# Kernel optimization log

Measured on AMD Instinct MI355X. Metric: run time of the kernel, lower is better.

Reference implementation:

```python
import jax, jax.numpy as jnp
import numpy as np

DIM = 512  # word_hidden_size * 2


def _linear_params(key, din, dout, scale=0.05):
    kw, kb = jax.random.split(key)
    W = jax.random.normal(kw, (din, dout), dtype=jnp.float32) * scale
    b = jax.random.normal(kb, (dout,), dtype=jnp.float32) * scale
    return W, b


def setup_inputs() -> dict:
    key = jax.random.key(0)
    ks = jax.random.split(key, 16)
    S_c, S_q, B = 256, 32, 32
    inp = {
        'context_output': jax.random.normal(ks[0], (S_c, B, DIM), dtype=jnp.float32),
        'question_output': jax.random.normal(ks[1], (S_q, B, DIM), dtype=jnp.float32),
        'question_hidden_state': jax.random.normal(ks[2], (B, DIM), dtype=jnp.float32),
        'image_output': jax.random.normal(ks[3], (S_c, B, DIM), dtype=jnp.float32),
    }
    names = ['fc1', 'fc2', 'dm', 'rm', 'qm', 'rr', 'rg', 'qg']
    for i, n in enumerate(names):
        W, b = _linear_params(ks[4 + i], DIM, DIM)
        inp['W_' + n] = W
        inp['b_' + n] = b
    W_ms, b_ms = _linear_params(ks[12], DIM, 1)
    inp['W_ms'] = W_ms
    inp['b_ms'] = b_ms
    return inp


def reference(context_output, question_output, question_hidden_state, image_output,
              W_fc1, b_fc1, W_fc2, b_fc2, W_dm, b_dm, W_rm, b_rm, W_qm, b_qm,
              W_rr, b_rr, W_rg, b_rg, W_qg, b_qg, W_ms, b_ms):
    # ctx: [B, S, D] = fc1(context) + fc2(image) after seq-first -> batch-first permute
    ctx = (jnp.einsum('sbd,de->bse', context_output, W_fc1) + b_fc1
           + jnp.einsum('sbd,de->bse', image_output, W_fc2) + b_fc2)
    # hoist loop-invariant linear_dm(ctx): same math, computed once
    ctx_dm = jnp.einsum('bsd,de->bse', ctx, W_dm) + b_dm  # [B, S, D]

    B = ctx.shape[0]
    r0 = jnp.zeros((B, DIM), dtype=ctx.dtype)

    def step(r, q_t):  # r: [B, D], q_t: [B, D]
        rm = r @ W_rm + b_rm          # [B, D]
        qm = q_t @ W_qm + b_qm        # [B, D]
        m = jnp.tanh(ctx_dm + rm[:, None, :] + qm[:, None, :])  # [B, S, D]
        logits = jnp.einsum('bsd,do->bso', m, W_ms)[..., 0] + b_ms[0]  # [B, S]
        s = jax.nn.softmax(logits, axis=1)                     # [B, S]
        r_new = jnp.einsum('bs,bsd->bd', s, ctx) + jnp.tanh(r @ W_rr + b_rr)
        return r_new, None

    r, _ = jax.lax.scan(step, r0, question_output)  # scan over question tokens

    g = (r @ W_rg + b_rg) + (question_hidden_state @ W_qg + b_qg)  # [B, D]
    return g
```

## Files before the change

### kernel.cpp

```cpp
#include <hip/hip_runtime.h>
#include <hip/hip_bf16.h>

#define DIMD 512
#define NB   32
#define NS   256
#define NT   32
#define SA_STR  66
#define SCT_STR 258
#define SR_STR  132

typedef __bf16 bf16x8 __attribute__((ext_vector_type(8)));
typedef float  f32x4  __attribute__((ext_vector_type(4)));
typedef unsigned long long u64;

__device__ __forceinline__ float tanh_fast(float x) {
    float e = __expf(2.f * x);
    return 1.f - 2.f / (e + 1.f);
}

__device__ __forceinline__ void gl_lds16(const __bf16* g, __bf16* l) {
    __builtin_amdgcn_global_load_lds((const __attribute__((address_space(1))) void*)g,
                                     (__attribute__((address_space(3))) void*)l, 16, 0, 0);
}

__device__ __forceinline__ void pub64(u64* p, float v, unsigned tag) {
    u64 pk = ((u64)__float_as_uint(v) << 32) | (u64)tag;
    __hip_atomic_store(p, pk, __ATOMIC_RELAXED, __HIP_MEMORY_SCOPE_AGENT);
}
__device__ __forceinline__ float poll64(const u64* p, unsigned tag) {
    u64 v = __hip_atomic_load(p, __ATOMIC_RELAXED, __HIP_MEMORY_SCOPE_AGENT);
    while ((unsigned)v != tag) {
        __builtin_amdgcn_s_sleep(1);
        v = __hip_atomic_load(p, __ATOMIC_RELAXED, __HIP_MEMORY_SCOPE_AGENT);
    }
    return __uint_as_float((unsigned)(v >> 32));
}

__global__ void k_prep_all(const float* __restrict__ ctxin, const float* __restrict__ img,
                           const float* __restrict__ qin,
                           const float* __restrict__ Wfc1, const float* __restrict__ Wfc2,
                           const float* __restrict__ Wdm, const float* __restrict__ Wqm,
                           const float* __restrict__ Wrm, const float* __restrict__ Wrr,
                           const float* __restrict__ Wrg, const float* __restrict__ Wqg,
                           __bf16* __restrict__ acat, __bf16* __restrict__ qp,
                           __bf16* __restrict__ wcatT, __bf16* __restrict__ wdmT,
                           __bf16* __restrict__ wqmT, __bf16* __restrict__ wrmT,
                           __bf16* __restrict__ wrrT, __bf16* __restrict__ wrgT,
                           __bf16* __restrict__ wqgT) {
    int row = blockIdx.x;
    if (row < 8192) {
        int b = row >> 8, s = row & 255;
        const float* c  = ctxin + ((size_t)s * NB + b) * DIMD;
        const float* im = img   + ((size_t)s * NB + b) * DIMD;
        __bf16* o = acat + (size_t)row * 1024;
        for (int d = threadIdx.x; d < DIMD; d += 256) {
            o[d]       = (__bf16)c[d];
            o[512 + d] = (__bf16)im[d];
        }
    } else if (row < 10240) {
        int idx = (row - 8192) * 256 + threadIdx.x;
        qp[idx] = (__bf16)qin[idx];
    } else {
        __shared__ float tile[32][33];
        int zz = (row - 10240) >> 8;
        int idx = (row - 10240) & 255;
        int bx = idx & 15, by = idx >> 4;
        int x = threadIdx.x & 31, y = threadIdx.x >> 5;
        const float* src = (zz == 0) ? Wfc1 : (zz == 1) ? Wfc2 : (zz == 2) ? Wdm
                         : (zz == 3) ? Wqm : (zz == 4) ? Wrm : (zz == 5) ? Wrr
                         : (zz == 6) ? Wrg : Wqg;
        __bf16* dst; int stride, off;
        if (zz < 2) { dst = wcatT; stride = 1024; off = zz * 512; }
        else {
            dst = (zz == 2) ? wdmT : (zz == 3) ? wqmT : (zz == 4) ? wrmT
                : (zz == 5) ? wrrT : (zz == 6) ? wrgT : wqgT;
            stride = 512; off = 0;
        }
        int c0 = bx * 32, r0 = by * 32;
#pragma unroll
        for (int k = 0; k < 32; k += 8)
            tile[y + k][x] = src[(size_t)(r0 + y + k) * DIMD + c0 + x];
        __syncthreads();
#pragma unroll
        for (int k = 0; k < 32; k += 8)
            dst[(size_t)(c0 + y + k) * stride + off + r0 + x] = (__bf16)tile[x][y + k];
    }
}

__device__ __forceinline__ void gemm_tile(const __bf16* __restrict__ A,
                                          const __bf16* __restrict__ BT,
                                          const float* __restrict__ bias1,
                                          const float* __restrict__ bias2,
                                          void* __restrict__ out, int N, int K,
                                          int m0, int n0, int out_f32,
                                          __bf16* As, __bf16* Bs) {
    int tid = threadIdx.x, wave = tid >> 6, lane = tid & 63;
    int wm = wave >> 1, wn = wave & 1;
    int lr = lane & 15, lq = lane >> 4;

    f32x4 acc[2][2];
#pragma unroll
    for (int i = 0; i < 2; i++)
#pragma unroll
        for (int j = 0; j < 2; j++) acc[i][j] = (f32x4){0.f, 0.f, 0.f, 0.f};

    int g0 = (wave * 2 + 0) * 64 + lane;
    int g1 = (wave * 2 + 1) * 64 + lane;
    int r0_ = g0 >> 3, c0_ = g0 & 7;
    int r1_ = g1 >> 3, c1_ = g1 & 7;
    __bf16* la0 = As + (wave * 2 + 0) * 512;
    __bf16* la1 = As + (wave * 2 + 1) * 512;
    __bf16* lb0 = Bs + (wave * 2 + 0) * 512;
    __bf16* lb1 = Bs + (wave * 2 + 1) * 512;

    for (int kk = 0; kk < K; kk += 64) {
        gl_lds16(A  + (size_t)(m0 + r0_) * K + kk + c0_ * 8, la0);
        gl_lds16(A  + (size_t)(m0 + r1_) * K + kk + c1_ * 8, la1);
        gl_lds16(BT + (size_t)(n0 + r0_) * K + kk + c0_ * 8, lb0);
        gl_lds16(BT + (size_t)(n0 + r1_) * K + kk + c1_ * 8, lb1);
        __syncthreads();
#pragma unroll
        for (int k2 = 0; k2 < 64; k2 += 32) {
            bf16x8 af[2], bfv[2];
#pragma unroll
            for (int i = 0; i < 2; i++)
                af[i] = *(const bf16x8*)(As + (wm * 32 + i * 16 + lr) * 64 + k2 + lq * 8);
#pragma unroll
            for (int j = 0; j < 2; j++)
                bfv[j] = *(const bf16x8*)(Bs + (wn * 32 + j * 16 + lr) * 64 + k2 + lq * 8);
#pragma unroll
            for (int i = 0; i < 2; i++)
#pragma unroll
                for (int j = 0; j < 2; j++)
                    acc[i][j] = __builtin_amdgcn_mfma_f32_16x16x32_bf16(af[i], bfv[j], acc[i][j], 0, 0, 0);
        }
        __syncthreads();
    }

#pragma unroll
    for (int i = 0; i < 2; i++)
#pragma unroll
        for (int j = 0; j < 2; j++) {
            int col = n0 + wn * 32 + j * 16 + lr;
            float bs = (bias1 ? bias1[col] : 0.f) + (bias2 ? bias2[col] : 0.f);
#pragma unroll
            for (int r = 0; r < 4; r++) {
                int row = m0 + wm * 32 + i * 16 + lq * 4 + r;
                float v = acc[i][j][r] + bs;
                if (out_f32) ((float*)out)[(size_t)row * N + col] = v;
                else         ((__bf16*)out)[(size_t)row * N + col] = (__bf16)v;
            }
        }
}

__global__ void k_gemm64(const __bf16* __restrict__ A, const __bf16* __restrict__ BT,
                         const float* __restrict__ bias1, const float* __restrict__ bias2,
                         void* __restrict__ out, int M, int N, int K, int out_f32) {
    __shared__ __bf16 As[64 * 64];
    __shared__ __bf16 Bs[64 * 64];
    gemm_tile(A, BT, bias1, bias2, out, N, K, blockIdx.x * 64, blockIdx.y * 64, out_f32, As, Bs);
}

__global__ void k_fused(const __bf16* __restrict__ ctxb, const __bf16* __restrict__ wdmT,
                        const float* __restrict__ bdm, __bf16* __restrict__ ctxdm,
                        const __bf16* __restrict__ qp, const __bf16* __restrict__ wqmT,
                        const float* __restrict__ bqm, float* __restrict__ qmf,
                        __bf16* __restrict__ ctxT) {
    __shared__ __bf16 As[64 * 64];
    __shared__ __bf16 Bs[64 * 64];
    int bid = blockIdx.x;
    if (bid < 1024) {
        gemm_tile(ctxb, wdmT, bdm, nullptr, ctxdm, 512, 512,
                  (bid & 127) * 64, (bid >> 7) * 64, 0, As, Bs);
    } else if (bid < 1152) {
        int b2 = bid - 1024;
        gemm_tile(qp, wqmT, bqm, nullptr, qmf, 512, 512,
                  (b2 & 15) * 64, (b2 >> 4) * 64, 1, As, Bs);
    } else {
        int b3 = bid - 1152;
        int z = b3 >> 7, rest = b3 & 127;
        int c0 = (rest & 15) * 32, s0 = (rest >> 4) * 32;
        __bf16* tile = As;
        int x = threadIdx.x & 31, y = threadIdx.x >> 5;
        const __bf16* S = ctxb + (size_t)z * NS * DIMD;
        __bf16* D = ctxT + (size_t)z * DIMD * NS;
#pragma unroll
        for (int k = 0; k < 32; k += 8)
            tile[(y + k) * 33 + x] = S[(size_t)(s0 + y + k) * DIMD + c0 + x];
        __syncthreads();
#pragma unroll
        for (int k = 0; k < 32; k += 8)
            D[(size_t)(c0 + y + k) * NS + s0 + x] = tile[x * 33 + y + k];
    }
}

__global__ __launch_bounds__(512, 2) void k_scan(
    const __bf16* __restrict__ ctxdm,
    const __bf16* __restrict__ ctxT,
    const __bf16* __restrict__ wrmT,
    const __bf16* __restrict__ wrrT,
    const float* __restrict__ qmf,
    const float* __restrict__ wms, const float* __restrict__ brm,
    const float* __restrict__ brr,
    u64* parts,
    u64* rpub,
    float* __restrict__ rbuf) {
    int bid = blockIdx.x;
    int b = bid & 31, j = bid >> 5;
    int tid = threadIdx.x, wave = tid >> 6, lane = tid & 63;
    int g = lane >> 3, i = lane & 7;

    __shared__ __bf16 sA[256 * SA_STR];
    __shared__ __bf16 sCT[64 * SCT_STR];
    __shared__ float  sQ[NT * 64];
    __shared__ float  sq[512];
    __shared__ float  sp[256];
    __shared__ float  s4[4];
    __shared__ float  sps[8 * 68];
    __shared__ float  srm[64], sh[64];
    __shared__ float  sr4[4 * SR_STR];
    __shared__ float  smv[512];

    for (int c = tid; c < 2048; c += 512) {
        int row = c >> 3, c8 = c & 7;
        *(bf16x8*)(sA + row * SA_STR + c8 * 8) =
            *(const bf16x8*)(ctxdm + ((size_t)(b * NS + row)) * DIMD + j * 64 + c8 * 8);
    }
    for (int c = tid; c < 2048; c += 512) {
        int col = c >> 5, s8 = c & 31;
        *(bf16x8*)(sCT + col * SCT_STR + s8 * 8) =
            *(const bf16x8*)(ctxT + ((size_t)(b * DIMD) + j * 64 + col) * NS + s8 * 8);
    }
    for (int c = tid; c < NT * 64; c += 512) {
        int tt = c >> 6, e = c & 63;
        sQ[c] = qmf[((size_t)tt * NB + b) * DIMD + j * 64 + e];
    }
    int m = tid >> 8, cl = (tid >> 2) & 63, q = tid & 3;
    const __bf16* wp = (m ? wrrT : wrmT) + ((size_t)(j * 64 + cl)) * DIMD + q * 128;
    bf16x8 wreg[16];
#pragma unroll
    for (int u = 0; u < 16; u++) wreg[u] = *(const bf16x8*)(wp + u * 8);

    float wm[8];
#pragma unroll
    for (int u = 0; u < 8; u++) wm[u] = wms[j * 64 + i * 8 + u];
    if (tid < 64) {
        srm[tid] = brm[j * 64 + tid];
        sh[tid]  = tanh_fast(brr[j * 64 + tid]);
    }
    __syncthreads();

    for (int t = 0; t < NT; t++) {
        unsigned tag = (unsigned)(t + 1);
        float rq[8];
#pragma unroll
        for (int u = 0; u < 8; u++) rq[u] = srm[i * 8 + u] + sQ[t * 64 + i * 8 + u];
#pragma unroll
        for (int k = 0; k < 4; k++) {
            int s = wave * 32 + k * 8 + g;
            bf16x8 cv = *(const bf16x8*)(sA + s * SA_STR + i * 8);
            float a = 0.f;
#pragma unroll
            for (int u = 0; u < 8; u++)
                a += tanh_fast((float)cv[u] + rq[u]) * wm[u];
            a += __shfl_xor(a, 1); a += __shfl_xor(a, 2); a += __shfl_xor(a, 4);
            if (i == 0) pub64(&parts[(b * 8 + j) * NS + s], a, tag);
        }

        {
            int s = tid >> 1, jh = (tid & 1) * 4;
            const u64* p0 = &parts[(b * 8 + jh + 0) * NS + s];
            const u64* p1 = &parts[(b * 8 + jh + 1) * NS + s];
            const u64* p2 = &parts[(b * 8 + jh + 2) * NS + s];
            const u64* p3 = &parts[(b * 8 + jh + 3) * NS + s];
            u64 v0, v1, v2, v3;
            for (;;) {
                v0 = __hip_atomic_load(p0, __ATOMIC_RELAXED, __HIP_MEMORY_SCOPE_AGENT);
                v1 = __hip_atomic_load(p1, __ATOMIC_RELAXED, __HIP_MEMORY_SCOPE_AGENT);
                v2 = __hip_atomic_load(p2, __ATOMIC_RELAXED, __HIP_MEMORY_SCOPE_AGENT);
                v3 = __hip_atomic_load(p3, __ATOMIC_RELAXED, __HIP_MEMORY_SCOPE_AGENT);
                if ((unsigned)v0 == tag && (unsigned)v1 == tag &&
                    (unsigned)v2 == tag && (unsigned)v3 == tag) break;
                __builtin_amdgcn_s_sleep(1);
            }
            sq[tid] = __uint_as_float((unsigned)(v0 >> 32)) + __uint_as_float((unsigned)(v1 >> 32))
                    + __uint_as_float((unsigned)(v2 >> 32)) + __uint_as_float((unsigned)(v3 >> 32));
        }
        __syncthreads();
        float ev = 0.f;
        if (tid < NS) { ev = __expf(sq[2 * tid] + sq[2 * tid + 1]); sp[tid] = ev; }
#pragma unroll
        for (int off = 32; off; off >>= 1) ev += __shfl_xor(ev, off);
        if (tid < NS && lane == 0) s4[wave] = ev;
        __syncthreads();
        float inv = 1.f / (s4[0] + s4[1] + s4[2] + s4[3]);
        {
            const __bf16* cp = sCT + lane * SCT_STR + wave * 32;
            const float* pp = sp + wave * 32;
            float a = 0.f;
#pragma unroll
            for (int k = 0; k < 32; k += 8) {
                bf16x8 v = *(const bf16x8*)(cp + k);
#pragma unroll
                for (int u = 0; u < 8; u++) a = fmaf(pp[k + u], (float)v[u], a);
            }
            sps[wave * 68 + lane] = a;
        }
        __syncthreads();
        if (tid < 64) {
            float a = 0.f;
#pragma unroll
            for (int w2 = 0; w2 < 8; w2++) a += sps[w2 * 68 + tid];
            float rv = a * inv + sh[tid];
            if (t == NT - 1) rbuf[b * DIMD + j * 64 + tid] = rv;
            else             pub64(&rpub[b * DIMD + j * 64 + tid], rv, tag);
        }
        if (t == NT - 1) break;

        sr4[(tid >> 7) * SR_STR + (tid & 127)] = poll64(&rpub[b * DIMD + tid], tag);
        __syncthreads();
        {
            const float* sv = sr4 + q * SR_STR;
            float a0 = 0.f, a1 = 0.f;
#pragma unroll
            for (int u = 0; u < 16; u += 2) {
                bf16x8 w0 = wreg[u], w1 = wreg[u + 1];
#pragma unroll
                for (int e = 0; e < 8; e++) {
                    a0 = fmaf(sv[u * 8 + e],     (float)w0[e], a0);
                    a1 = fmaf(sv[u * 8 + 8 + e], (float)w1[e], a1);
                }
            }
            smv[tid] = a0 + a1;
        }
        __syncthreads();
        if (tid < 128) {
            int m2 = tid >> 6, cl3 = tid & 63;
            float a = smv[m2 * 256 + cl3 * 4] + smv[m2 * 256 + cl3 * 4 + 1]
                    + smv[m2 * 256 + cl3 * 4 + 2] + smv[m2 * 256 + cl3 * 4 + 3];
            int col = j * 64 + cl3;
            if (m2 == 0) srm[cl3] = a + brm[col];
            else         sh[cl3]  = tanh_fast(a + brr[col]);
        }
        __syncthreads();
    }
}

__global__ void k_final2(const float* __restrict__ r, const float* __restrict__ qh,
                         const __bf16* __restrict__ wrgT, const __bf16* __restrict__ wqgT,
                         const float* __restrict__ brg, const float* __restrict__ bqg,
                         float* __restrict__ out) {
    int clx = threadIdx.x & 7, b = threadIdx.x >> 3;
    int col = blockIdx.x * 8 + clx;
    const __bf16* w1 = wrgT + (size_t)col * DIMD;
    const __bf16* w2 = wqgT + (size_t)col * DIMD;
    const float* rp = r + (size_t)b * DIMD;
    const float* qp = qh + (size_t)b * DIMD;
    float acc = brg[col] + bqg[col];
#pragma unroll 4
    for (int d = 0; d < DIMD; d += 8) {
        bf16x8 a = *(const bf16x8*)(w1 + d);
        bf16x8 c = *(const bf16x8*)(w2 + d);
#pragma unroll
        for (int u = 0; u < 8; u++)
            acc += rp[d + u] * (float)a[u] + qp[d + u] * (float)c[u];
    }
    out[b * DIMD + col] = acc;
}


extern "C" void kernel_launch(void* const* d_in, const int* in_sizes, int n_in,
                              void* d_out, int out_size, void* d_ws, size_t ws_size,
                              hipStream_t stream) {
    const float* ctx_in = (const float*)d_in[0];
    const float* q_in   = (const float*)d_in[1];
    const float* qh     = (const float*)d_in[2];
    const float* img    = (const float*)d_in[3];
    const float* W_fc1  = (const float*)d_in[4];
    const float* b_fc1  = (const float*)d_in[5];
    const float* W_fc2  = (const float*)d_in[6];
    const float* b_fc2  = (const float*)d_in[7];
    const float* W_dm   = (const float*)d_in[8];
    const float* b_dm   = (const float*)d_in[9];
    const float* W_rm   = (const float*)d_in[10];
    const float* b_rm   = (const float*)d_in[11];
    const float* W_qm   = (const float*)d_in[12];
    const float* b_qm   = (const float*)d_in[13];
    const float* W_rr   = (const float*)d_in[14];
    const float* b_rr   = (const float*)d_in[15];
    const float* W_rg   = (const float*)d_in[16];
    const float* b_rg   = (const float*)d_in[17];
    const float* W_qg   = (const float*)d_in[18];
    const float* b_qg   = (const float*)d_in[19];
    const float* W_ms   = (const float*)d_in[20];

    char* w = (char*)d_ws;
    __bf16* acat  = (__bf16*)w;  w += (size_t)8192 * 1024 * 2;
    __bf16* qp    = (__bf16*)w;  w += (size_t)1024 * 512 * 2;
    __bf16* wcatT = (__bf16*)w;  w += (size_t)512 * 1024 * 2;
    __bf16* wdmT  = (__bf16*)w;  w += (size_t)512 * 512 * 2;
    __bf16* wqmT  = (__bf16*)w;  w += (size_t)512 * 512 * 2;
    __bf16* wrmT  = (__bf16*)w;  w += (size_t)512 * 512 * 2;
    __bf16* wrrT  = (__bf16*)w;  w += (size_t)512 * 512 * 2;
    __bf16* wrgT  = (__bf16*)w;  w += (size_t)512 * 512 * 2;
    __bf16* wqgT  = (__bf16*)w;  w += (size_t)512 * 512 * 2;
    __bf16* ctxb  = (__bf16*)w;  w += (size_t)8192 * 512 * 2;
    __bf16* ctxdm = (__bf16*)w;  w += (size_t)8192 * 512 * 2;
    char* x = (char*)acat;
    __bf16* ctxT  = (__bf16*)x;  x += (size_t)NB * DIMD * NS * 2;
    float*  qmf   = (float*)x;   x += (size_t)1024 * 512 * 4;
    u64*    rpub  = (u64*)x;     x += (size_t)NB * DIMD * 8;
    u64*    parts = (u64*)x;     x += (size_t)NB * 8 * NS * 8;
    float*  rbuf  = (float*)x;   x += (size_t)NB * DIMD * 4;

    k_prep_all<<<12288, 256, 0, stream>>>(ctx_in, img, q_in, W_fc1, W_fc2, W_dm,
                                          W_qm, W_rm, W_rr, W_rg, W_qg, acat, qp,
                                          wcatT, wdmT, wqmT, wrmT, wrrT, wrgT, wqgT);
    k_gemm64<<<dim3(128, 8), 256, 0, stream>>>(acat, wcatT, b_fc1, b_fc2, ctxb, 8192, 512, 1024, 0);
    k_fused<<<5248, 256, 0, stream>>>(ctxb, wdmT, b_dm, ctxdm, qp, wqmT, b_qm, qmf, ctxT);
    k_scan<<<256, 512, 0, stream>>>(ctxdm, ctxT, wrmT, wrrT, qmf, W_ms,
                                    b_rm, b_rr, parts, rpub, rbuf);
    k_final2<<<64, 256, 0, stream>>>(rbuf, qh, wrgT, wqgT, b_rg, b_qg, (float*)d_out);
}
```

Baseline: 447.7 us.

## Use 128x128 GEMM tiles and fold final gate projection into scan kernel

GEMM tiles grow from 64x64 (K step 64) to 128x128 (K step 32), so each wave does 4x4 MFMA blocks. This raises operand reuse per LDS load and cuts the block count for the fc and dm/qm GEMMs. Separately, the last scan step now publishes r and computes the rg/qg output projection inside k_scan, which removes the k_final2 launch and the round-trip through rbuf. The cost is more registers per thread for the accumulators, fewer blocks (256 for the main GEMM) to fill the CUs, and extra weight loads in the scan's final step.

```diff
diff --git a/kernel.cpp b/kernel.cpp
--- a/kernel.cpp
+++ b/kernel.cpp
@@ -87,65 +87,62 @@
     }
 }
 
-__device__ __forceinline__ void gemm_tile(const __bf16* __restrict__ A,
-                                          const __bf16* __restrict__ BT,
-                                          const float* __restrict__ bias1,
-                                          const float* __restrict__ bias2,
-                                          void* __restrict__ out, int N, int K,
-                                          int m0, int n0, int out_f32,
-                                          __bf16* As, __bf16* Bs) {
+__device__ __forceinline__ void gemm_tile128(const __bf16* __restrict__ A,
+                                             const __bf16* __restrict__ BT,
+                                             const float* __restrict__ bias1,
+                                             const float* __restrict__ bias2,
+                                             void* __restrict__ out, int N, int K,
+                                             int m0, int n0, int out_f32,
+                                             __bf16* As, __bf16* Bs) {
     int tid = threadIdx.x, wave = tid >> 6, lane = tid & 63;
-    int wm = wave >> 1, wn = wave & 1;
+    int wm_ = wave >> 1, wn = wave & 1;
     int lr = lane & 15, lq = lane >> 4;
 
-    f32x4 acc[2][2];
-#pragma unroll
-    for (int i = 0; i < 2; i++)
-#pragma unroll
-        for (int j = 0; j < 2; j++) acc[i][j] = (f32x4){0.f, 0.f, 0.f, 0.f};
+    f32x4 acc[4][4];
+#pragma unroll
+    for (int i = 0; i < 4; i++)
+#pragma unroll
+        for (int j = 0; j < 4; j++) acc[i][j] = (f32x4){0.f, 0.f, 0.f, 0.f};
 
     int g0 = (wave * 2 + 0) * 64 + lane;
     int g1 = (wave * 2 + 1) * 64 + lane;
-    int r0_ = g0 >> 3, c0_ = g0 & 7;
-    int r1_ = g1 >> 3, c1_ = g1 & 7;
+    int r0_ = g0 >> 2, c0_ = g0 & 3;
+    int r1_ = g1 >> 2, c1_ = g1 & 3;
     __bf16* la0 = As + (wave * 2 + 0) * 512;
     __bf16* la1 = As + (wave * 2 + 1) * 512;
     __bf16* lb0 = Bs + (wave * 2 + 0) * 512;
     __bf16* lb1 = Bs + (wave * 2 + 1) * 512;
 
-    for (int kk = 0; kk < K; kk += 64) {
+    for (int kk = 0; kk < K; kk += 32) {
         gl_lds16(A  + (size_t)(m0 + r0_) * K + kk + c0_ * 8, la0);
         gl_lds16(A  + (size_t)(m0 + r1_) * K + kk + c1_ * 8, la1);
         gl_lds16(BT + (size_t)(n0 + r0_) * K + kk + c0_ * 8, lb0);
         gl_lds16(BT + (size_t)(n0 + r1_) * K + kk + c1_ * 8, lb1);
         __syncthreads();
-#pragma unroll
-        for (int k2 = 0; k2 < 64; k2 += 32) {
-            bf16x8 af[2], bfv[2];
-#pragma unroll
-            for (int i = 0; i < 2; i++)
-                af[i] = *(const bf16x8*)(As + (wm * 32 + i * 16 + lr) * 64 + k2 + lq * 8);
-#pragma unroll
-            for (int j = 0; j < 2; j++)
-                bfv[j] = *(const bf16x8*)(Bs + (wn * 32 + j * 16 + lr) * 64 + k2 + lq * 8);
-#pragma unroll
-            for (int i = 0; i < 2; i++)
-#pragma unroll
-                for (int j = 0; j < 2; j++)
-                    acc[i][j] = __builtin_amdgcn_mfma_f32_16x16x32_bf16(af[i], bfv[j], acc[i][j], 0, 0, 0);
-        }
-        __syncthreads();
-    }
-
-#pragma unroll
-    for (int i = 0; i < 2; i++)
-#pragma unroll
-        for (int j = 0; j < 2; j++) {
-            int col = n0 + wn * 32 + j * 16 + lr;
+        bf16x8 af[4], bfv[4];
+#pragma unroll
+        for (int i = 0; i < 4; i++)
+            af[i] = *(const bf16x8*)(As + (wm_ * 64 + i * 16 + lr) * 32 + lq * 8);
+#pragma unroll
+        for (int j = 0; j < 4; j++)
+            bfv[j] = *(const bf16x8*)(Bs + (wn * 64 + j * 16 + lr) * 32 + lq * 8);
+#pragma unroll
+        for (int i = 0; i < 4; i++)
+#pragma unroll
+            for (int j = 0; j < 4; j++)
+                acc[i][j] = __builtin_amdgcn_mfma_f32_16x16x32_bf16(af[i], bfv[j], acc[i][j], 0, 0, 0);
+        __syncthreads();
+    }
+
+#pragma unroll
+    for (int i = 0; i < 4; i++)
+#pragma unroll
+        for (int j = 0; j < 4; j++) {
+            int col = n0 + wn * 64 + j * 16 + lr;
             float bs = (bias1 ? bias1[col] : 0.f) + (bias2 ? bias2[col] : 0.f);
 #pragma unroll
             for (int r = 0; r < 4; r++) {
-                int row = m0 + wm * 32 + i * 16 + lq * 4 + r;
+                int row = m0 + wm_ * 64 + i * 16 + lq * 4 + r;
                 float v = acc[i][j][r] + bs;
                 if (out_f32) ((float*)out)[(size_t)row * N + col] = v;
                 else         ((__bf16*)out)[(size_t)row * N + col] = (__bf16)v;
@@ -153,12 +150,12 @@
         }
 }
 
-__global__ void k_gemm64(const __bf16* __restrict__ A, const __bf16* __restrict__ BT,
-                         const float* __restrict__ bias1, const float* __restrict__ bias2,
-                         void* __restrict__ out, int M, int N, int K, int out_f32) {
-    __shared__ __bf16 As[64 * 64];
-    __shared__ __bf16 Bs[64 * 64];
-    gemm_tile(A, BT, bias1, bias2, out, N, K, blockIdx.x * 64, blockIdx.y * 64, out_f32, As, Bs);
+__global__ void k_gemm128(const __bf16* __restrict__ A, const __bf16* __restrict__ BT,
+                          const float* __restrict__ bias1, const float* __restrict__ bias2,
+                          void* __restrict__ out, int M, int N, int K, int out_f32) {
+    __shared__ __bf16 As[128 * 32];
+    __shared__ __bf16 Bs[128 * 32];
+    gemm_tile128(A, BT, bias1, bias2, out, N, K, blockIdx.x * 128, blockIdx.y * 128, out_f32, As, Bs);
 }
 
 __global__ void k_fused(const __bf16* __restrict__ ctxb, const __bf16* __restrict__ wdmT,
@@ -166,18 +163,18 @@
                         const __bf16* __restrict__ qp, const __bf16* __restrict__ wqmT,
                         const float* __restrict__ bqm, float* __restrict__ qmf,
                         __bf16* __restrict__ ctxT) {
-    __shared__ __bf16 As[64 * 64];
-    __shared__ __bf16 Bs[64 * 64];
+    __shared__ __bf16 As[128 * 32];
+    __shared__ __bf16 Bs[128 * 32];
     int bid = blockIdx.x;
-    if (bid < 1024) {
-        gemm_tile(ctxb, wdmT, bdm, nullptr, ctxdm, 512, 512,
-                  (bid & 127) * 64, (bid >> 7) * 64, 0, As, Bs);
-    } else if (bid < 1152) {
-        int b2 = bid - 1024;
-        gemm_tile(qp, wqmT, bqm, nullptr, qmf, 512, 512,
-                  (b2 & 15) * 64, (b2 >> 4) * 64, 1, As, Bs);
+    if (bid < 256) {
+        gemm_tile128(ctxb, wdmT, bdm, nullptr, ctxdm, 512, 512,
+                     (bid & 63) * 128, (bid >> 6) * 128, 0, As, Bs);
+    } else if (bid < 288) {
+        int b2 = bid - 256;
+        gemm_tile128(qp, wqmT, bqm, nullptr, qmf, 512, 512,
+                     (b2 & 7) * 128, (b2 >> 3) * 128, 1, As, Bs);
     } else {
-        int b3 = bid - 1152;
+        int b3 = bid - 288;
         int z = b3 >> 7, rest = b3 & 127;
         int c0 = (rest & 15) * 32, s0 = (rest >> 4) * 32;
         __bf16* tile = As;
@@ -202,9 +199,13 @@
     const float* __restrict__ qmf,
     const float* __restrict__ wms, const float* __restrict__ brm,
     const float* __restrict__ brr,
+    const float* __restrict__ qh,
+    const __bf16* __restrict__ wrgT,
+    const __bf16* __restrict__ wqgT,
+    const float* __restrict__ brg, const float* __restrict__ bqg,
     u64* parts,
     u64* rpub,
-    float* __restrict__ rbuf) {
+    float* __restrict__ out) {
     int bid = blockIdx.x;
     int b = bid & 31, j = bid >> 5;
     int tid = threadIdx.x, wave = tid >> 6, lane = tid & 63;
@@ -219,6 +220,7 @@
     __shared__ float  sps[8 * 68];
     __shared__ float  srm[64], sh[64];
     __shared__ float  sr4[4 * SR_STR];
+    __shared__ float  sqh4[4 * SR_STR];
     __shared__ float  smv[512];
 
     for (int c = tid; c < 2048; c += 512) {
@@ -235,6 +237,7 @@
         int tt = c >> 6, e = c & 63;
         sQ[c] = qmf[((size_t)tt * NB + b) * DIMD + j * 64 + e];
     }
+    sqh4[(tid >> 7) * SR_STR + (tid & 127)] = qh[(size_t)b * DIMD + tid];
     int m = tid >> 8, cl = (tid >> 2) & 63, q = tid & 3;
     const __bf16* wp = (m ? wrrT : wrmT) + ((size_t)(j * 64 + cl)) * DIMD + q * 128;
     bf16x8 wreg[16];
@@ -312,14 +315,12 @@
 #pragma unroll
             for (int w2 = 0; w2 < 8; w2++) a += sps[w2 * 68 + tid];
             float rv = a * inv + sh[tid];
-            if (t == NT - 1) rbuf[b * DIMD + j * 64 + tid] = rv;
-            else             pub64(&rpub[b * DIMD + j * 64 + tid], rv, tag);
-        }
-        if (t == NT - 1) break;
+            pub64(&rpub[b * DIMD + j * 64 + tid], rv, tag);
+        }
 
         sr4[(tid >> 7) * SR_STR + (tid & 127)] = poll64(&rpub[b * DIMD + tid], tag);
         __syncthreads();
-        {
+        if (t < NT - 1) {
             const float* sv = sr4 + q * SR_STR;
             float a0 = 0.f, a1 = 0.f;
 #pragma unroll
@@ -332,40 +333,44 @@
                 }
             }
             smv[tid] = a0 + a1;
-        }
-        __syncthreads();
-        if (tid < 128) {
-            int m2 = tid >> 6, cl3 = tid & 63;
-            float a = smv[m2 * 256 + cl3 * 4] + smv[m2 * 256 + cl3 * 4 + 1]
-                    + smv[m2 * 256 + cl3 * 4 + 2] + smv[m2 * 256 + cl3 * 4 + 3];
-            int col = j * 64 + cl3;
-            if (m2 == 0) srm[cl3] = a + brm[col];
-            else         sh[cl3]  = tanh_fast(a + brr[col]);
-        }
-        __syncthreads();
-    }
-}
-
-__global__ void k_final2(const float* __restrict__ r, const float* __restrict__ qh,
-                         const __bf16* __restrict__ wrgT, const __bf16* __restrict__ wqgT,
-                         const float* __restrict__ brg, const float* __restrict__ bqg,
-                         float* __restrict__ out) {
-    int clx = threadIdx.x & 7, b = threadIdx.x >> 3;
-    int col = blockIdx.x * 8 + clx;
-    const __bf16* w1 = wrgT + (size_t)col * DIMD;
-    const __bf16* w2 = wqgT + (size_t)col * DIMD;
-    const float* rp = r + (size_t)b * DIMD;
-    const float* qp = qh + (size_t)b * DIMD;
-    float acc = brg[col] + bqg[col];
-#pragma unroll 4
-    for (int d = 0; d < DIMD; d += 8) {
-        bf16x8 a = *(const bf16x8*)(w1 + d);
-        bf16x8 c = *(const bf16x8*)(w2 + d);
-#pragma unroll
-        for (int u = 0; u < 8; u++)
-            acc += rp[d + u] * (float)a[u] + qp[d + u] * (float)c[u];
-    }
-    out[b * DIMD + col] = acc;
+            __syncthreads();
+            if (tid < 128) {
+                int m2 = tid >> 6, cl3 = tid & 63;
+                float a = smv[m2 * 256 + cl3 * 4] + smv[m2 * 256 + cl3 * 4 + 1]
+                        + smv[m2 * 256 + cl3 * 4 + 2] + smv[m2 * 256 + cl3 * 4 + 3];
+                int col = j * 64 + cl3;
+                if (m2 == 0) srm[cl3] = a + brm[col];
+                else         sh[cl3]  = tanh_fast(a + brr[col]);
+            }
+            __syncthreads();
+        } else {
+            const __bf16* wp2 = (m ? wqgT : wrgT) + ((size_t)(j * 64 + cl)) * DIMD + q * 128;
+            const float* sv = (m ? sqh4 : sr4) + q * SR_STR;
+            float a0 = 0.f, a1 = 0.f;
+#pragma unroll
+            for (int u = 0; u < 16; u += 2) {
+                bf16x8 w0 = *(const bf16x8*)(wp2 + u * 8);
+                bf16x8 w1 = *(const bf16x8*)(wp2 + u * 8 + 8);
+#pragma unroll
+                for (int e = 0; e < 8; e++) {
+                    a0 = fmaf(sv[u * 8 + e],     (float)w0[e], a0);
+                    a1 = fmaf(sv[u * 8 + 8 + e], (float)w1[e], a1);
+                }
+            }
+            smv[tid] = a0 + a1;
+            __syncthreads();
+            if (tid < 64) {
+                int col = j * 64 + tid;
+                float a = brg[col] + bqg[col];
+#pragma unroll
+                for (int m2 = 0; m2 < 2; m2++)
+#pragma unroll
+                    for (int q2 = 0; q2 < 4; q2++)
+                        a += smv[m2 * 256 + tid * 4 + q2];
+                out[(size_t)b * DIMD + col] = a;
+            }
+        }
+    }
 }
 
 
@@ -411,14 +416,13 @@
     float*  qmf   = (float*)x;   x += (size_t)1024 * 512 * 4;
     u64*    rpub  = (u64*)x;     x += (size_t)NB * DIMD * 8;
     u64*    parts = (u64*)x;     x += (size_t)NB * 8 * NS * 8;
-    float*  rbuf  = (float*)x;   x += (size_t)NB * DIMD * 4;
 
     k_prep_all<<<12288, 256, 0, stream>>>(ctx_in, img, q_in, W_fc1, W_fc2, W_dm,
                                           W_qm, W_rm, W_rr, W_rg, W_qg, acat, qp,
                                           wcatT, wdmT, wqmT, wrmT, wrrT, wrgT, wqgT);
-    k_gemm64<<<dim3(128, 8), 256, 0, stream>>>(acat, wcatT, b_fc1, b_fc2, ctxb, 8192, 512, 1024, 0);
-    k_fused<<<5248, 256, 0, stream>>>(ctxb, wdmT, b_dm, ctxdm, qp, wqmT, b_qm, qmf, ctxT);
+    k_gemm128<<<dim3(64, 4), 256, 0, stream>>>(acat, wcatT, b_fc1, b_fc2, ctxb, 8192, 512, 1024, 0);
+    k_fused<<<4384, 256, 0, stream>>>(ctxb, wdmT, b_dm, ctxdm, qp, wqmT, b_qm, qmf, ctxT);
     k_scan<<<256, 512, 0, stream>>>(ctxdm, ctxT, wrmT, wrrT, qmf, W_ms,
-                                    b_rm, b_rr, parts, rpub, rbuf);
-    k_final2<<<64, 256, 0, stream>>>(rbuf, qh, wrgT, wqgT, b_rg, b_qg, (float*)d_out);
-}
+                                    b_rm, b_rr, qh, wrgT, wqgT, b_rg, b_qg,
+                                    parts, rpub, (float*)d_out);
+}
```

After: 433.6 us. 1.03x faster.
